# Kernel tuning notes

Measured on AMD Instinct MI355X. Metric: run time of the kernel, lower is better.

The kernel has to match this reference:

```python
import jax, jax.numpy as jnp
import numpy as np

B, C, H, W = 32, 256, 64, 64
S, K = 128, 8  # NUM_CHANNEL_SETS, MAX_CHANNELS_PER_SET


def setup_inputs() -> dict:
    key = jax.random.key(0)
    kx, ki = jax.random.split(key)
    x = jax.random.normal(kx, (B, C, H, W), dtype=jnp.float32)
    channel_idx_sets = jax.random.randint(ki, (S, K), 0, C, dtype=jnp.int32)
    return {"x": x, "channel_idx_sets": channel_idx_sets}


def reference(x, channel_idx_sets):
    # Gather channels for each set, then max-reduce over the set dimension.
    # x: [B, C, H, W]; channel_idx_sets: [S, K] int32 -> out: [B, S, H, W]
    gathered = x[:, channel_idx_sets, :, :]  # [B, S, K, H, W]
    return jnp.max(gathered, axis=2)
```

## Files before the change

kernel.cpp:

```cpp
#include <hip/hip_runtime.h>


constexpr int Bb = 32, Cc = 256, Hh = 64, Ww = 64, Ss = 128, Kk = 8;
constexpr int HW4 = (Hh * Ww) / 4;

__global__ __launch_bounds__(256) void fmp_kernel(
    const float4* __restrict__ x4,
    const int*    __restrict__ idx,
    float4*       __restrict__ out4)
{
    const int gid = blockIdx.x * 256 + threadIdx.x;
    const int hw4 = gid & (HW4 - 1);
    const int s   = (blockIdx.x >> 2) & (Ss - 1);
    const int b   =  blockIdx.x >> 9;

    const int* __restrict__ ip = idx + s * Kk;
    const float4* __restrict__ xb = x4 + (size_t)b * (Cc * HW4) + hw4;

    float4 m = xb[(size_t)ip[0] * HW4];
    #pragma unroll
    for (int k = 1; k < Kk; ++k) {
        const float4 v = xb[(size_t)ip[k] * HW4];
        m.x = fmaxf(m.x, v.x);
        m.y = fmaxf(m.y, v.y);
        m.z = fmaxf(m.z, v.z);
        m.w = fmaxf(m.w, v.w);
    }
    out4[gid] = m;
}

extern "C" void kernel_launch(void* const* d_in, const int* in_sizes, int n_in,
                              void* d_out, int out_size, void* d_ws, size_t ws_size,
                              hipStream_t stream) {
    const float4* x4  = (const float4*)d_in[0];
    const int*    idx = (const int*)d_in[1];
    float4*       o4  = (float4*)d_out;

    const int n4     = Bb * Ss * Hh * Ww / 4;
    const int blocks = n4 / 256;
    fmp_kernel<<<blocks, 256, 0, stream>>>(x4, idx, o4);
}
```

Baseline: 209.5 us.

## Stage all channels of a spatial tile in LDS and gather-max from shared memory

Each block now loads a 16-float4 spatial tile for all 256 channels of one batch into LDS (64 KB), along with the full index table, then computes all 128 set maxima from LDS. Each input element is read from global memory once instead of once per set that references it. The cost is a large LDS footprint that limits occupancy, fewer blocks (2048), and short 256-byte row segments on the global loads.

```diff
diff --git a/kernel.cpp b/kernel.cpp
--- a/kernel.cpp
+++ b/kernel.cpp
@@ -3,30 +3,51 @@
 
 constexpr int Bb = 32, Cc = 256, Hh = 64, Ww = 64, Ss = 128, Kk = 8;
 constexpr int HW4 = (Hh * Ww) / 4;
+constexpr int T4  = 16;
+constexpr int NT  = HW4 / T4;
 
-__global__ __launch_bounds__(256) void fmp_kernel(
+__global__ __launch_bounds__(256, 2) void fmp_kernel(
     const float4* __restrict__ x4,
     const int*    __restrict__ idx,
     float4*       __restrict__ out4)
 {
-    const int gid = blockIdx.x * 256 + threadIdx.x;
-    const int hw4 = gid & (HW4 - 1);
-    const int s   = (blockIdx.x >> 2) & (Ss - 1);
-    const int b   =  blockIdx.x >> 9;
+    __shared__ float4 lx[Cc * T4];
+    __shared__ int4   lidx4[Ss * Kk / 4];
 
-    const int* __restrict__ ip = idx + s * Kk;
-    const float4* __restrict__ xb = x4 + (size_t)b * (Cc * HW4) + hw4;
+    const int tid  = threadIdx.x;
+    const int tile = blockIdx.x & (NT - 1);
+    const int b    = blockIdx.x >> 6;
 
-    float4 m = xb[(size_t)ip[0] * HW4];
+    lidx4[tid] = ((const int4*)idx)[tid];
+
+    const float4* __restrict__ xb = x4 + (size_t)b * (Cc * HW4) + tile * T4;
     #pragma unroll
-    for (int k = 1; k < Kk; ++k) {
-        const float4 v = xb[(size_t)ip[k] * HW4];
-        m.x = fmaxf(m.x, v.x);
-        m.y = fmaxf(m.y, v.y);
-        m.z = fmaxf(m.z, v.z);
-        m.w = fmaxf(m.w, v.w);
+    for (int i = 0; i < 16; ++i) {
+        const int flat = i * 256 + tid;
+        const int c    = flat >> 4;
+        const int tt   = flat & (T4 - 1);
+        lx[flat] = xb[(size_t)c * HW4 + tt];
     }
-    out4[gid] = m;
+    __syncthreads();
+
+    const int t = tid & (T4 - 1);
+    float4* __restrict__ op = out4 + (size_t)b * (Ss * HW4) + tile * T4 + t;
+
+#define FMAX4(m, c) { const float4 v = lx[(c) * T4 + t];          \
+        m.x = fmaxf(m.x, v.x); m.y = fmaxf(m.y, v.y);             \
+        m.z = fmaxf(m.z, v.z); m.w = fmaxf(m.w, v.w); }
+
+    #pragma unroll
+    for (int pass = 0; pass < 8; ++pass) {
+        const int s   = pass * 16 + (tid >> 4);
+        const int4 i0 = lidx4[s * 2];
+        const int4 i1 = lidx4[s * 2 + 1];
+        float4 m = lx[i0.x * T4 + t];
+        FMAX4(m, i0.y); FMAX4(m, i0.z); FMAX4(m, i0.w);
+        FMAX4(m, i1.x); FMAX4(m, i1.y); FMAX4(m, i1.z); FMAX4(m, i1.w);
+        op[(size_t)s * HW4] = m;
+    }
+#undef FMAX4
 }
 
 extern "C" void kernel_launch(void* const* d_in, const int* in_sizes, int n_in,
@@ -36,7 +57,6 @@
     const int*    idx = (const int*)d_in[1];
     float4*       o4  = (float4*)d_out;
 
-    const int n4     = Bb * Ss * Hh * Ww / 4;
-    const int blocks = n4 / 256;
+    const int blocks = Bb * NT;
     fmp_kernel<<<blocks, 256, 0, stream>>>(x4, idx, o4);
 }
```

Result: no change. 211.3 us (+0.9%).
